# Kernel optimization log

Measured on AMD Instinct MI355X. Metric: run time of the kernel, lower is better.

The kernel has to match this reference:

```python
import jax, jax.numpy as jnp
import numpy as np

N_HEADS = 16


def setup_inputs() -> dict:
    key = jax.random.key(0)
    ks = jax.random.split(key, 5)
    B, T, C = 4, 2048, 1024
    return {
        "x": jax.random.normal(ks[0], (B, T, C), dtype=jnp.float32),
        "W_qkv": jax.random.normal(ks[1], (C, 3 * C), dtype=jnp.float32) * 0.02,
        "b_qkv": jax.random.normal(ks[2], (3 * C,), dtype=jnp.float32) * 0.02,
        "W_proj": jax.random.normal(ks[3], (C, C), dtype=jnp.float32) * 0.02,
        "b_proj": jax.random.normal(ks[4], (C,), dtype=jnp.float32) * 0.02,
    }


def reference(x, W_qkv, b_qkv, W_proj, b_proj):
    B, T, C = x.shape
    H = N_HEADS
    hs = C // H
    # QKV projection. NOTE: original reshapes (B,T,3C) -> (B,T,H,3*hs) then
    # chunks last dim, so q/k/v are interleaved per-head slices of the output.
    qkv = x @ W_qkv + b_qkv                       # [B, T, 3C]
    qkv = qkv.reshape(B, T, H, 3 * hs).transpose(0, 2, 1, 3)  # [B, H, T, 3*hs]
    q, k, v = jnp.split(qkv, 3, axis=-1)          # each [B, H, T, hs]
    scale = 1.0 / (hs ** 0.5)
    scores = jnp.einsum("bhqd,bhkd->bhqk", q, k) * scale  # [B, H, T, T]
    causal = jnp.tril(jnp.ones((T, T), dtype=bool))
    scores = jnp.where(causal, scores, jnp.float32(-1e9))
    attn = jax.nn.softmax(scores, axis=-1)
    out = jnp.einsum("bhqk,bhkd->bhqd", attn, v)  # [B, H, T, hs]
    out = out.transpose(0, 2, 1, 3).reshape(B, T, C)
    return out @ W_proj + b_proj
```

## Files before the change

kernel.cpp:

```cpp
#include <hip/hip_runtime.h>

typedef unsigned short u16;
typedef unsigned int u32;
typedef __attribute__((ext_vector_type(8))) short short8;
typedef __attribute__((ext_vector_type(8))) unsigned short u16x8;
typedef __attribute__((ext_vector_type(4))) unsigned short u16x4;
typedef __attribute__((ext_vector_type(2))) unsigned int u32x2;
typedef __attribute__((ext_vector_type(4))) float f32x4;

__device__ __forceinline__ u16 f2bf(float f){
  u32 u = __builtin_bit_cast(u32, f);
  u32 r = u + 0x7FFFu + ((u >> 16) & 1u);
  return (u16)(r >> 16);
}
__device__ __forceinline__ float bf2f(u16 h){
  u32 u = ((u32)h) << 16;
  return __builtin_bit_cast(float, u);
}
__device__ __forceinline__ float f3max(float a, float b, float c){
  return fmaxf(a, fmaxf(b, c));
}
__device__ __forceinline__ u32 cvtpk(float lo, float hi){
  u32 r;
  asm("v_cvt_pk_bf16_f32 %0, %1, %2" : "=v"(r) : "v"(lo), "v"(hi));
  return r;
}

__device__ __forceinline__ void gld_lds16(const u16* g, u16* l){
  __builtin_amdgcn_global_load_lds(
      (const __attribute__((address_space(1))) u32*)g,
      (__attribute__((address_space(3))) u32*)l, 16, 0, 0);
}

#define MFMA(a,b,c) __builtin_amdgcn_mfma_f32_16x16x32_bf16((a),(b),(c),0,0,0)

__global__ void k_cast_x(const float* __restrict__ in, u16* __restrict__ out, int n8){
  int i = blockIdx.x*256 + threadIdx.x;
  if (i >= n8) return;
  const float4 a = ((const float4*)in)[2*i];
  const float4 b = ((const float4*)in)[2*i+1];
  u16x8 o;
  o[0]=f2bf(a.x); o[1]=f2bf(a.y); o[2]=f2bf(a.z); o[3]=f2bf(a.w);
  o[4]=f2bf(b.x); o[5]=f2bf(b.y); o[6]=f2bf(b.z); o[7]=f2bf(b.w);
  ((u16x8*)out)[i] = o;
}

__global__ void k_transpose_cast(const float* __restrict__ in, u16* __restrict__ out,
                                 int R, int C){
  __shared__ float tile[32][33];
  int c0 = blockIdx.x*32, r0 = blockIdx.y*32;
  int tx = threadIdx.x, ty = threadIdx.y;
  #pragma unroll
  for (int i=0;i<4;i++) tile[ty+8*i][tx] = in[(size_t)(r0+ty+8*i)*C + c0+tx];
  __syncthreads();
  #pragma unroll
  for (int i=0;i<4;i++) out[(size_t)(c0+ty+8*i)*R + r0+tx] = f2bf(tile[tx][ty+8*i]);
}

#define GS_A(T_, BUF) do{                                                      \
  size_t k0_ = (size_t)(T_)*64;                                                \
  _Pragma("unroll")                                                            \
  for (int l=0;l<2;l++){                                                       \
    int r_ = l*64 + (tid>>3);                                                  \
    gld_lds16(Ag + (size_t)(brow + r_)*1024 + k0_ + (((tid&7)^(r_&7))*8),      \
              &Alds[(BUF)*8192 + l*4096 + tid*8]);                             \
  }                                                                            \
}while(0)

#define GS_B(T_, BUF, H_) do{                                                  \
  size_t k0_ = (size_t)(T_)*64;                                                \
  _Pragma("unroll")                                                            \
  for (int l=0;l<2;l++){                                                       \
    int r_ = (H_)*128 + l*64 + (tid>>3);                                       \
    gld_lds16(Bg + (size_t)(bcol + r_)*1024 + k0_ + (((tid&7)^(r_&7))*8),      \
              &Blds[(BUF)*16384 + (H_)*8192 + l*4096 + tid*8]);                \
  }                                                                            \
}while(0)

#define RD_A(MQ, CUR) do{                                                      \
  _Pragma("unroll")                                                            \
  for (int m=0;m<2;m++)                                                        \
    _Pragma("unroll")                                                          \
    for (int k=0;k<2;k++){                                                     \
      int hr = wr*64 + (MQ)*32 + m*16 + lr16;                                  \
      af[(MQ)*2+m][k] = *(const short8*)&Alds[(CUR)*8192 + hr*64 + (((k*4+lg)^(hr&7))*8)]; \
    }                                                                          \
}while(0)

#define RD_B(NQ, CUR) do{                                                      \
  _Pragma("unroll")                                                            \
  for (int n=0;n<2;n++)                                                        \
    _Pragma("unroll")                                                          \
    for (int k=0;k<2;k++){                                                     \
      int hr = wc*64 + (NQ)*32 + n*16 + lr16;                                  \
      bfv[(NQ)*2+n][k] = *(const short8*)&Blds[(CUR)*16384 + hr*64 + (((k*4+lg)^(hr&7))*8)]; \
    }                                                                          \
}while(0)

#define MF8(MQ, NQ)                                                            \
  _Pragma("unroll")                                                            \
  for (int k=0;k<2;k++)                                                        \
    _Pragma("unroll")                                                          \
    for (int m=0;m<2;m++)                                                      \
      _Pragma("unroll")                                                        \
      for (int n=0;n<2;n++)                                                    \
        acc[(MQ)*2+m][(NQ)*2+n] = MFMA(af[(MQ)*2+m][k], bfv[(NQ)*2+n][k], acc[(MQ)*2+m][(NQ)*2+n]);

#define G_TILE(T_, CUR, PF) do{                                                \
  RD_A(0, CUR); RD_B(0, CUR);                                                  \
  if (PF) GS_A((T_)+1, (CUR)^1);                                               \
  __builtin_amdgcn_s_barrier();                                                \
  __builtin_amdgcn_s_setprio(1); MF8(0,0); __builtin_amdgcn_s_setprio(0);      \
  __builtin_amdgcn_s_barrier();                                                \
  RD_B(1, CUR);                                                                \
  if (PF) GS_B((T_)+1, (CUR)^1, 0);                                            \
  __builtin_amdgcn_s_barrier();                                                \
  __builtin_amdgcn_s_setprio(1); MF8(0,1); __builtin_amdgcn_s_setprio(0);      \
  __builtin_amdgcn_s_barrier();                                                \
  RD_A(1, CUR);                                                                \
  if (PF) GS_B((T_)+1, (CUR)^1, 1);                                            \
  __builtin_amdgcn_s_barrier();                                                \
  __builtin_amdgcn_s_setprio(1); MF8(1,1); __builtin_amdgcn_s_setprio(0);      \
  __builtin_amdgcn_s_barrier();                                                \
  __builtin_amdgcn_s_setprio(1); MF8(1,0); __builtin_amdgcn_s_setprio(0);      \
  asm volatile("s_waitcnt vmcnt(0)" ::: "memory");                             \
  __builtin_amdgcn_sched_barrier(0);                                           \
  __builtin_amdgcn_s_barrier();                                                \
}while(0)

template<int OUT_BF16>
__global__ __launch_bounds__(512, 2) void gemm_ph(const u16* __restrict__ Ag,
                                                  const u16* __restrict__ Bg,
                                                  const float* __restrict__ bias,
                                                  void* __restrict__ Cp, int N){
  extern __shared__ u16 lds[];
  u16* Alds = lds;
  u16* Blds = lds + 16384;
  int tid = threadIdx.x, lane = tid&63, wid = tid>>6;
  int wr = wid>>2, wc = wid&3;
  int lr16 = lane&15, lg = lane>>4;
  int nbx = gridDim.x;
  int nwg = nbx*gridDim.y;
  int lin = blockIdx.y*nbx + blockIdx.x;
  int cpx = nwg>>3;
  int swz = (lin&7)*cpx + (lin>>3);
  int bx = swz % nbx, by = swz / nbx;
  size_t brow = (size_t)by*128, bcol = (size_t)bx*256;
  f32x4 acc[4][4] = {};
  short8 af[4][2], bfv[4][2];

  GS_A(0, 0);
  GS_B(0, 0, 0);
  GS_B(0, 0, 1);
  __syncthreads();

  #pragma unroll 1
  for (int kt=0; kt<16; kt+=2){
    G_TILE(kt,   0, true);
    G_TILE(kt+1, 1, (kt+2<16));
  }

  #pragma unroll
  for (int ni=0;ni<4;ni++){
    size_t col = bcol + wc*64 + ni*16 + lr16;
    float bs = bias[col];
    #pragma unroll
    for (int mi=0;mi<4;mi++)
      #pragma unroll
      for (int j=0;j<4;j++){
        size_t row = brow + wr*64 + mi*16 + lg*4 + j;
        float v = acc[mi][ni][j] + bs;
        if (OUT_BF16) ((u16*)Cp)[row*(size_t)N + col] = f2bf(v);
        else          ((float*)Cp)[row*(size_t)N + col] = v;
      }
  }
}

#define ATTN_ITER(KB, CUR, PF) do{                                             \
  int kv0 = (KB)*64;                                                           \
  if (PF){                                                                     \
    int kv1 = kv0 + 64;                                                        \
    va[0] = *(const u16x4*)(qkv + (bt0 + kv1 + vr0    )*3072 + hq + 128 + vd0);\
    va[1] = *(const u16x4*)(qkv + (bt0 + kv1 + vr0 + 1)*3072 + hq + 128 + vd0);\
    gld_lds16(qkv + (bt0+kv1+kr)*3072 + hq + 64 + kcs, &Ks[(CUR)^1][tid*8]);   \
  }                                                                            \
  f32x4 st[4];                                                                 \
  __builtin_amdgcn_s_setprio(1);                                               \
  _Pragma("unroll")                                                            \
  for (int s=0;s<4;s++){                                                       \
    short8 kf0 = *(const short8*)&Ks[CUR][(s*16+lr16)*64 + ((lg  )^rx)*8];     \
    short8 kf1 = *(const short8*)&Ks[CUR][(s*16+lr16)*64 + ((4+lg)^rx)*8];     \
    f32x4 z = {0,0,0,0};                                                       \
    z = MFMA(kf0, qf[0], z);                                                   \
    z = MFMA(kf1, qf[1], z);                                                   \
    st[s] = z;                                                                 \
  }                                                                            \
  __builtin_amdgcn_s_setprio(0);                                               \
  if (kv0 >= qbase){                                                           \
    _Pragma("unroll")                                                          \
    for (int s=0;s<4;s++)                                                      \
      _Pragma("unroll")                                                        \
      for (int j=0;j<4;j++){                                                   \
        int kvg = kv0 + s*16 + lg*4 + j;                                       \
        if (kvg > qglob) st[s][j] = -1e30f;                                    \
      }                                                                        \
  }                                                                            \
  {                                                                            \
    float mx = f3max(st[0][0], st[0][1], st[0][2]);                            \
    mx = f3max(mx, st[0][3], st[1][0]);                                        \
    mx = f3max(mx, st[1][1], st[1][2]);                                        \
    mx = f3max(mx, st[1][3], st[2][0]);                                        \
    mx = f3max(mx, st[2][1], st[2][2]);                                        \
    mx = f3max(mx, st[2][3], st[3][0]);                                        \
    mx = f3max(mx, st[3][1], st[3][2]);                                        \
    mx = fmaxf(mx, st[3][3]);                                                  \
    mx = fmaxf(mx, __shfl_xor(mx, 16));                                        \
    mx = fmaxf(mx, __shfl_xor(mx, 32));                                        \
    if (__any(mx > m_run + 8.f)){                                              \
      float m_new = fmaxf(m_run, mx);                                          \
      float al = exp2f(m_run - m_new);                                         \
      m_run = m_new;                                                           \
      float arow[4];                                                           \
      _Pragma("unroll")                                                        \
      for (int j=0;j<4;j++) arow[j] = __shfl(al, lg*4 + j);                    \
      _Pragma("unroll")                                                        \
      for (int db=0;db<4;db++)                                                 \
        _Pragma("unroll")                                                      \
        for (int j=0;j<4;j++) O[db][j] *= arow[j];                             \
      _Pragma("unroll")                                                        \
      for (int j=0;j<4;j++) acc_l[j] *= arow[j];                               \
    }                                                                          \
    float mr = m_run;                                                          \
    u32 pw[8];                                                                 \
    _Pragma("unroll")                                                          \
    for (int s=0;s<4;s++){                                                     \
      float p0 = exp2f(st[s][0]-mr), p1 = exp2f(st[s][1]-mr);                  \
      float p2 = exp2f(st[s][2]-mr), p3 = exp2f(st[s][3]-mr);                  \
      pw[s*2+0] = cvtpk(p0,p1);                                                \
      pw[s*2+1] = cvtpk(p2,p3);                                                \
    }                                                                          \
    _Pragma("unroll")                                                          \
    for (int s=0;s<4;s++){                                                     \
      int cp = (s*2 + (lg>>1)) ^ rx;                                           \
      u32x2 w2; w2[0] = pw[s*2]; w2[1] = pw[s*2+1];                            \
      *(u32x2*)&Pl[wv][lr16*64 + cp*8 + (lg&1)*4] = w2;                        \
    }                                                                          \
  }                                                                            \
  if (PF){                                                                     \
    _Pragma("unroll")                                                          \
    for (int k=0;k<4;k++){                                                     \
      int d = vd0+k;                                                           \
      int c = (vr0>>3) ^ (d&7) ^ ((d>>3)&7);                                   \
      u32 w = (u32)va[0][k] | ((u32)va[1][k]<<16);                             \
      *(u32*)&Vt[(CUR)^1][d*64 + c*8 + (vr0&7)] = w;                           \
    }                                                                          \
  }                                                                            \
  __builtin_amdgcn_s_setprio(1);                                               \
  _Pragma("unroll")                                                            \
  for (int B=0;B<2;B++){                                                       \
    short8 pa = *(const short8*)&Pl[wv][lr16*64 + (((B<<2)+lg)^rx)*8];         \
    acc_l = MFMA(pa, onesf, acc_l);                                            \
    _Pragma("unroll")                                                          \
    for (int db=0;db<4;db++){                                                  \
      int d = db*16 + lr16;                                                    \
      short8 vf = *(const short8*)&Vt[CUR][d*64 + ((((B<<2)+lg)^(d&7))^((d>>3)&7))*8]; \
      O[db] = MFMA(pa, vf, O[db]);                                             \
    }                                                                          \
  }                                                                            \
  __builtin_amdgcn_s_setprio(0);                                               \
  __syncthreads();                                                             \
}while(0)

__global__ __launch_bounds__(512, 4) void k_attn(const u16* __restrict__ qkv,
                                                 u16* __restrict__ o, int T){
  __shared__ __align__(16) u16 Ks[2][64*64];
  __shared__ __align__(16) u16 Vt[2][64*64];
  __shared__ __align__(16) u16 Pl[8][16*64];
  int tid = threadIdx.x, lane = tid&63, wv = tid>>6;
  int bh = blockIdx.x;
  int b = bh>>4, h = bh&15;
  int hq = h*192;
  size_t bt0 = (size_t)b*T;
  int lr16 = lane&15, lg = lane>>4;
  int rx = lr16&7;
  int vr0 = (tid>>4)*2, vd0 = (tid&15)*4;
  int kr  = tid>>3;
  int kcs = ((tid&7) ^ (kr&7))*8;
  u16x4 va[2];
  const float QS = 0.18033688f;
  u16x8 ov;
  #pragma unroll
  for (int j=0;j<8;j++) ov[j] = 0x3F80;
  const short8 onesf = __builtin_bit_cast(short8, ov);

  #pragma unroll 1
  for (int half=0; half<2; ++half){
    int qt = half ? (int)blockIdx.y : 15 - (int)blockIdx.y;
    int qbase = qt*128;
    short8 qf[2];
    {
      const u16* qp = qkv + (bt0 + qbase + wv*16 + lr16)*3072 + hq + lg*8;
      #pragma unroll
      for (int t=0;t<2;t++){
        u16x8 v = *(const u16x8*)(qp + t*32);
        #pragma unroll
        for (int j=0;j<8;j++) v[j] = f2bf(bf2f(v[j])*QS);
        qf[t] = __builtin_bit_cast(short8, v);
      }
    }
    f32x4 O[4] = {};
    f32x4 acc_l = {0,0,0,0};
    float m_run = -1e30f;
    int qglob = qbase + wv*16 + lr16;

    {
      va[0] = *(const u16x4*)(qkv + (bt0 + vr0    )*3072 + hq + 128 + vd0);
      va[1] = *(const u16x4*)(qkv + (bt0 + vr0 + 1)*3072 + hq + 128 + vd0);
      gld_lds16(qkv + (bt0+kr)*3072 + hq + 64 + kcs, &Ks[0][tid*8]);
      #pragma unroll
      for (int k=0;k<4;k++){
        int d = vd0+k;
        int c = (vr0>>3) ^ (d&7) ^ ((d>>3)&7);
        u32 w = (u32)va[0][k] | ((u32)va[1][k]<<16);
        *(u32*)&Vt[0][d*64 + c*8 + (vr0&7)] = w;
      }
    }
    __syncthreads();

    int nkv = 2*qt + 2;
    #pragma unroll 1
    for (int kb=0; kb<nkv; kb+=2){
      ATTN_ITER(kb,   0, true);
      ATTN_ITER(kb+1, 1, (kb+2<nkv));
    }
    {
      float lrow[4];
      #pragma unroll
      for (int j=0;j<4;j++) lrow[j] = __builtin_amdgcn_rcpf(acc_l[j]);
      #pragma unroll
      for (int db=0;db<4;db++)
        #pragma unroll
        for (int j=0;j<4;j++){
          size_t row = bt0 + qbase + wv*16 + lg*4 + j;
          o[row*1024 + h*64 + db*16 + lr16] = f2bf(O[db][j] * lrow[j]);
        }
    }
  }
}

extern "C" void kernel_launch(void* const* d_in, const int* in_sizes, int n_in,
                              void* d_out, int out_size, void* d_ws, size_t ws_size,
                              hipStream_t stream){
  (void)in_sizes; (void)n_in; (void)out_size; (void)ws_size;
  const float* x     = (const float*)d_in[0];
  const float* Wqkv  = (const float*)d_in[1];
  const float* bqkv  = (const float*)d_in[2];
  const float* Wproj = (const float*)d_in[3];
  const float* bproj = (const float*)d_in[4];
  float* out = (float*)d_out;
  const int B=4, T=2048, C=1024;
  const int M = B*T;
  char* ws = (char*)d_ws;
  u16* qkvb   = (u16*)(ws);
  u16* attnb  = (u16*)(ws + 50331648);
  u16* xb     = (u16*)(ws + 67108864);
  u16* wqkvT  = (u16*)(ws + 83886080);
  u16* wprojT = (u16*)(ws + 90177536);

  k_cast_x<<<4096, 256, 0, stream>>>(x, xb, M*C/8);
  dim3 tb(32,8);
  k_transpose_cast<<<dim3(96,32), tb, 0, stream>>>(Wqkv, wqkvT, C, 3*C);
  k_transpose_cast<<<dim3(32,32), tb, 0, stream>>>(Wproj, wprojT, C, C);
  gemm_ph<1><<<dim3(12,64), 512, 98304, stream>>>(xb, wqkvT, bqkv, qkvb, 3*C);
  k_attn<<<dim3(64,8), 512, 0, stream>>>(qkvb, attnb, T);
  gemm_ph<0><<<dim3(4,64), 512, 98304, stream>>>(attnb, wprojT, bproj, out, C);
}
```

Before: 183.1 us.

## Fuse x fp32-to-bf16 cast into QKV GEMM and widen attention KV tiles

```diff
diff --git a/kernel.cpp b/kernel.cpp
--- a/kernel.cpp
+++ b/kernel.cpp
@@ -6,6 +6,7 @@
 typedef __attribute__((ext_vector_type(8))) unsigned short u16x8;
 typedef __attribute__((ext_vector_type(4))) unsigned short u16x4;
 typedef __attribute__((ext_vector_type(2))) unsigned int u32x2;
+typedef __attribute__((ext_vector_type(4))) unsigned int u32x4;
 typedef __attribute__((ext_vector_type(4))) float f32x4;
 
 __device__ __forceinline__ u16 f2bf(float f){
@@ -33,17 +34,6 @@
 }
 
 #define MFMA(a,b,c) __builtin_amdgcn_mfma_f32_16x16x32_bf16((a),(b),(c),0,0,0)
-
-__global__ void k_cast_x(const float* __restrict__ in, u16* __restrict__ out, int n8){
-  int i = blockIdx.x*256 + threadIdx.x;
-  if (i >= n8) return;
-  const float4 a = ((const float4*)in)[2*i];
-  const float4 b = ((const float4*)in)[2*i+1];
-  u16x8 o;
-  o[0]=f2bf(a.x); o[1]=f2bf(a.y); o[2]=f2bf(a.z); o[3]=f2bf(a.w);
-  o[4]=f2bf(b.x); o[5]=f2bf(b.y); o[6]=f2bf(b.z); o[7]=f2bf(b.w);
-  ((u16x8*)out)[i] = o;
-}
 
 __global__ void k_transpose_cast(const float* __restrict__ in, u16* __restrict__ out,
                                  int R, int C){
@@ -62,8 +52,28 @@
   _Pragma("unroll")                                                            \
   for (int l=0;l<2;l++){                                                       \
     int r_ = l*64 + (tid>>3);                                                  \
-    gld_lds16(Ag + (size_t)(brow + r_)*1024 + k0_ + (((tid&7)^(r_&7))*8),      \
-              &Alds[(BUF)*8192 + l*4096 + tid*8]);                             \
+    size_t off_ = (size_t)(brow + r_)*1024 + k0_ + (((tid&7)^(r_&7))*8);       \
+    if (A_F32){                                                                \
+      fva[l*2]   = *(const float4*)(Agf + off_);                               \
+      fva[l*2+1] = *(const float4*)(Agf + off_ + 4);                           \
+    } else {                                                                   \
+      gld_lds16(Agu + off_, &Alds[(BUF)*8192 + l*4096 + tid*8]);               \
+    }                                                                          \
+  }                                                                            \
+}while(0)
+
+#define GS_A_COMMIT(BUF) do{                                                   \
+  if (A_F32){                                                                  \
+    _Pragma("unroll")                                                          \
+    for (int l=0;l<2;l++){                                                     \
+      u32x4 wv4;                                                               \
+      wv4[0]=cvtpk(fva[l*2].x,  fva[l*2].y);                                   \
+      wv4[1]=cvtpk(fva[l*2].z,  fva[l*2].w);                                   \
+      wv4[2]=cvtpk(fva[l*2+1].x,fva[l*2+1].y);                                 \
+      wv4[3]=cvtpk(fva[l*2+1].z,fva[l*2+1].w);                                 \
+      *(u32x4*)&Alds[(BUF)*8192 + l*4096 + tid*8] = wv4;                       \
+    }                                                                          \
+    asm volatile("s_waitcnt lgkmcnt(0)" ::: "memory");                         \
   }                                                                            \
 }while(0)
 
@@ -124,18 +134,22 @@
   __builtin_amdgcn_s_barrier();                                                \
   __builtin_amdgcn_s_setprio(1); MF8(1,0); __builtin_amdgcn_s_setprio(0);      \
   asm volatile("s_waitcnt vmcnt(0)" ::: "memory");                             \
+  if (PF) GS_A_COMMIT((CUR)^1);                                                \
   __builtin_amdgcn_sched_barrier(0);                                           \
   __builtin_amdgcn_s_barrier();                                                \
 }while(0)
 
-template<int OUT_BF16>
-__global__ __launch_bounds__(512, 2) void gemm_ph(const u16* __restrict__ Ag,
+template<int OUT_BF16, int A_F32>
+__global__ __launch_bounds__(512, 2) void gemm_ph(const void* __restrict__ Ag,
                                                   const u16* __restrict__ Bg,
                                                   const float* __restrict__ bias,
                                                   void* __restrict__ Cp, int N){
   extern __shared__ u16 lds[];
   u16* Alds = lds;
   u16* Blds = lds + 16384;
+  const u16* Agu = (const u16*)Ag;
+  const float* Agf = (const float*)Ag;
+  float4 fva[4];
   int tid = threadIdx.x, lane = tid&63, wid = tid>>6;
   int wr = wid>>2, wc = wid&3;
   int lr16 = lane&15, lg = lane>>4;
@@ -152,6 +166,7 @@
   GS_A(0, 0);
   GS_B(0, 0, 0);
   GS_B(0, 0, 1);
+  GS_A_COMMIT(0);
   __syncthreads();
 
   #pragma unroll 1
@@ -176,33 +191,28 @@
   }
 }
 
-#define ATTN_ITER(KB, CUR, PF) do{                                             \
-  int kv0 = (KB)*64;                                                           \
-  if (PF){                                                                     \
-    int kv1 = kv0 + 64;                                                        \
-    va[0] = *(const u16x4*)(qkv + (bt0 + kv1 + vr0    )*3072 + hq + 128 + vd0);\
-    va[1] = *(const u16x4*)(qkv + (bt0 + kv1 + vr0 + 1)*3072 + hq + 128 + vd0);\
-    gld_lds16(qkv + (bt0+kv1+kr)*3072 + hq + 64 + kcs, &Ks[(CUR)^1][tid*8]);   \
-  }                                                                            \
+#define ATTN_SUB(S, CUR) do{                                                   \
   f32x4 st[4];                                                                 \
   __builtin_amdgcn_s_setprio(1);                                               \
   _Pragma("unroll")                                                            \
-  for (int s=0;s<4;s++){                                                       \
-    short8 kf0 = *(const short8*)&Ks[CUR][(s*16+lr16)*64 + ((lg  )^rx)*8];     \
-    short8 kf1 = *(const short8*)&Ks[CUR][(s*16+lr16)*64 + ((4+lg)^rx)*8];     \
+  for (int sb=0;sb<4;sb++){                                                    \
+    int row = (S)*64 + sb*16 + lr16;                                           \
+    short8 kf0 = *(const short8*)&Ks[CUR][row*64 + ((lg  )^rx)*8];             \
+    short8 kf1 = *(const short8*)&Ks[CUR][row*64 + ((4+lg)^rx)*8];             \
     f32x4 z = {0,0,0,0};                                                       \
     z = MFMA(kf0, qf[0], z);                                                   \
     z = MFMA(kf1, qf[1], z);                                                   \
-    st[s] = z;                                                                 \
+    st[sb] = z;                                                                \
   }                                                                            \
   __builtin_amdgcn_s_setprio(0);                                               \
+  int kv0 = kvt + (S)*64;                                                      \
   if (kv0 >= qbase){                                                           \
     _Pragma("unroll")                                                          \
-    for (int s=0;s<4;s++)                                                      \
+    for (int sb=0;sb<4;sb++)                                                   \
       _Pragma("unroll")                                                        \
       for (int j=0;j<4;j++){                                                   \
-        int kvg = kv0 + s*16 + lg*4 + j;                                       \
-        if (kvg > qglob) st[s][j] = -1e30f;                                    \
+        int kvg = kv0 + sb*16 + lg*4 + j;                                      \
+        if (kvg > qglob) st[sb][j] = -1e30f;                                   \
       }                                                                        \
   }                                                                            \
   {                                                                            \
@@ -233,48 +243,65 @@
     float mr = m_run;                                                          \
     u32 pw[8];                                                                 \
     _Pragma("unroll")                                                          \
-    for (int s=0;s<4;s++){                                                     \
-      float p0 = exp2f(st[s][0]-mr), p1 = exp2f(st[s][1]-mr);                  \
-      float p2 = exp2f(st[s][2]-mr), p3 = exp2f(st[s][3]-mr);                  \
-      pw[s*2+0] = cvtpk(p0,p1);                                                \
-      pw[s*2+1] = cvtpk(p2,p3);                                                \
-    }                                                                          \
-    _Pragma("unroll")                                                          \
-    for (int s=0;s<4;s++){                                                     \
-      int cp = (s*2 + (lg>>1)) ^ rx;                                           \
-      u32x2 w2; w2[0] = pw[s*2]; w2[1] = pw[s*2+1];                            \
+    for (int sb=0;sb<4;sb++){                                                  \
+      float p0 = exp2f(st[sb][0]-mr), p1 = exp2f(st[sb][1]-mr);                \
+      float p2 = exp2f(st[sb][2]-mr), p3 = exp2f(st[sb][3]-mr);                \
+      pw[sb*2+0] = cvtpk(p0,p1);                                               \
+      pw[sb*2+1] = cvtpk(p2,p3);                                               \
+    }                                                                          \
+    _Pragma("unroll")                                                          \
+    for (int sb=0;sb<4;sb++){                                                  \
+      int cp = (sb*2 + (lg>>1)) ^ rx;                                          \
+      u32x2 w2; w2[0] = pw[sb*2]; w2[1] = pw[sb*2+1];                          \
       *(u32x2*)&Pl[wv][lr16*64 + cp*8 + (lg&1)*4] = w2;                        \
     }                                                                          \
   }                                                                            \
+  __builtin_amdgcn_s_setprio(1);                                               \
+  _Pragma("unroll")                                                            \
+  for (int B=0;B<2;B++){                                                       \
+    short8 pa = *(const short8*)&Pl[wv][lr16*64 + (((B<<2)+lg)^rx)*8];         \
+    acc_l = MFMA(pa, onesf, acc_l);                                            \
+    _Pragma("unroll")                                                          \
+    for (int db=0;db<4;db++){                                                  \
+      int d = db*16 + lr16;                                                    \
+      short8 vf = *(const short8*)&Vt[d*128 + ((S)*8 + (((B<<2)+lg)^((d&7)^((d>>3)&7))))*8]; \
+      O[db] = MFMA(pa, vf, O[db]);                                             \
+    }                                                                          \
+  }                                                                            \
+  __builtin_amdgcn_s_setprio(0);                                               \
+}while(0)
+
+#define ATTN_TILE(T_, CUR, PF) do{                                             \
+  int kvt = (T_)*128;                                                          \
+  if (PF){                                                                     \
+    int kv1 = kvt + 128;                                                       \
+    _Pragma("unroll")                                                          \
+    for (int i=0;i<4;i++)                                                      \
+      va[i] = *(const u16x4*)(qkv + (bt0 + kv1 + vr0 + i)*3072 + hq + 128 + vd0); \
+    gld_lds16(qkv + (bt0+kv1+kr)*3072 + hq + 64 + kcs, &Ks[(CUR)^1][tid*8]);   \
+    gld_lds16(qkv + (bt0+kv1+64+kr)*3072 + hq + 64 + kcs, &Ks[(CUR)^1][4096 + tid*8]); \
+  }                                                                            \
+  ATTN_SUB(0, CUR);                                                            \
+  ATTN_SUB(1, CUR);                                                            \
+  __builtin_amdgcn_s_barrier();                                                \
   if (PF){                                                                     \
     _Pragma("unroll")                                                          \
     for (int k=0;k<4;k++){                                                     \
       int d = vd0+k;                                                           \
       int c = (vr0>>3) ^ (d&7) ^ ((d>>3)&7);                                   \
-      u32 w = (u32)va[0][k] | ((u32)va[1][k]<<16);                             \
-      *(u32*)&Vt[(CUR)^1][d*64 + c*8 + (vr0&7)] = w;                           \
-    }                                                                          \
-  }                                                                            \
-  __builtin_amdgcn_s_setprio(1);                                               \
-  _Pragma("unroll")                                                            \
-  for (int B=0;B<2;B++){                                                       \
-    short8 pa = *(const short8*)&Pl[wv][lr16*64 + (((B<<2)+lg)^rx)*8];         \
-    acc_l = MFMA(pa, onesf, acc_l);                                            \
-    _Pragma("unroll")                                                          \
-    for (int db=0;db<4;db++){                                                  \
-      int d = db*16 + lr16;                                                    \
-      short8 vf = *(const short8*)&Vt[CUR][d*64 + ((((B<<2)+lg)^(d&7))^((d>>3)&7))*8]; \
-      O[db] = MFMA(pa, vf, O[db]);                                             \
-    }                                                                          \
-  }                                                                            \
-  __builtin_amdgcn_s_setprio(0);                                               \
+      u32x2 w;                                                                 \
+      w[0] = (u32)va[0][k] | ((u32)va[1][k]<<16);                              \
+      w[1] = (u32)va[2][k] | ((u32)va[3][k]<<16);                              \
+      *(u32x2*)&Vt[d*128 + c*8 + (vr0&7)] = w;                                 \
+    }                                                                          \
+  }                                                                            \
   __syncthreads();                                                             \
 }while(0)
 
 __global__ __launch_bounds__(512, 4) void k_attn(const u16* __restrict__ qkv,
                                                  u16* __restrict__ o, int T){
-  __shared__ __align__(16) u16 Ks[2][64*64];
-  __shared__ __align__(16) u16 Vt[2][64*64];
+  __shared__ __align__(16) u16 Ks[2][128*64];
+  __shared__ __align__(16) u16 Vt[64*128];
   __shared__ __align__(16) u16 Pl[8][16*64];
   int tid = threadIdx.x, lane = tid&63, wv = tid>>6;
   int bh = blockIdx.x;
@@ -283,10 +310,10 @@
   size_t bt0 = (size_t)b*T;
   int lr16 = lane&15, lg = lane>>4;
   int rx = lr16&7;
-  int vr0 = (tid>>4)*2, vd0 = (tid&15)*4;
+  int vr0 = (tid>>4)*4, vd0 = (tid&15)*4;
   int kr  = tid>>3;
   int kcs = ((tid&7) ^ (kr&7))*8;
-  u16x4 va[2];
+  u16x4 va[4];
   const float QS = 0.18033688f;
   u16x8 ov;
   #pragma unroll
@@ -314,25 +341,32 @@
     int qglob = qbase + wv*16 + lr16;
 
     {
-      va[0] = *(const u16x4*)(qkv + (bt0 + vr0    )*3072 + hq + 128 + vd0);
-      va[1] = *(const u16x4*)(qkv + (bt0 + vr0 + 1)*3072 + hq + 128 + vd0);
+      #pragma unroll
+      for (int i=0;i<4;i++)
+        va[i] = *(const u16x4*)(qkv + (bt0 + vr0 + i)*3072 + hq + 128 + vd0);
       gld_lds16(qkv + (bt0+kr)*3072 + hq + 64 + kcs, &Ks[0][tid*8]);
+      gld_lds16(qkv + (bt0+64+kr)*3072 + hq + 64 + kcs, &Ks[0][4096 + tid*8]);
       #pragma unroll
       for (int k=0;k<4;k++){
         int d = vd0+k;
         int c = (vr0>>3) ^ (d&7) ^ ((d>>3)&7);
-        u32 w = (u32)va[0][k] | ((u32)va[1][k]<<16);
-        *(u32*)&Vt[0][d*64 + c*8 + (vr0&7)] = w;
+        u32x2 w;
+        w[0] = (u32)va[0][k] | ((u32)va[1][k]<<16);
+        w[1] = (u32)va[2][k] | ((u32)va[3][k]<<16);
+        *(u32x2*)&Vt[d*128 + c*8 + (vr0&7)] = w;
       }
     }
     __syncthreads();
 
-    int nkv = 2*qt + 2;
+    int nt = qt + 1;
+    int t = 0;
     #pragma unroll 1
-    for (int kb=0; kb<nkv; kb+=2){
-      ATTN_ITER(kb,   0, true);
-      ATTN_ITER(kb+1, 1, (kb+2<nkv));
+    for (; t+1 < nt; t += 2){
+      ATTN_TILE(t,   0, true);
+      ATTN_TILE(t+1, 1, (t+2<nt));
     }
+    if (t < nt) ATTN_TILE(t, 0, false);
+
     {
       float lrow[4];
       #pragma unroll
@@ -359,19 +393,17 @@
   const float* bproj = (const float*)d_in[4];
   float* out = (float*)d_out;
   const int B=4, T=2048, C=1024;
-  const int M = B*T;
+  (void)B;
   char* ws = (char*)d_ws;
   u16* qkvb   = (u16*)(ws);
   u16* attnb  = (u16*)(ws + 50331648);
-  u16* xb     = (u16*)(ws + 67108864);
   u16* wqkvT  = (u16*)(ws + 83886080);
   u16* wprojT = (u16*)(ws + 90177536);
 
-  k_cast_x<<<4096, 256, 0, stream>>>(x, xb, M*C/8);
   dim3 tb(32,8);
   k_transpose_cast<<<dim3(96,32), tb, 0, stream>>>(Wqkv, wqkvT, C, 3*C);
   k_transpose_cast<<<dim3(32,32), tb, 0, stream>>>(Wproj, wprojT, C, C);
-  gemm_ph<1><<<dim3(12,64), 512, 98304, stream>>>(xb, wqkvT, bqkv, qkvb, 3*C);
+  gemm_ph<1,1><<<dim3(12,64), 512, 98304, stream>>>((const void*)x, wqkvT, bqkv, qkvb, 3*C);
   k_attn<<<dim3(64,8), 512, 0, stream>>>(qkvb, attnb, T);
-  gemm_ph<0><<<dim3(4,64), 512, 98304, stream>>>(attnb, wprojT, bproj, out, C);
-}
+  gemm_ph<0,0><<<dim3(4,64), 512, 98304, stream>>>((const void*)attnb, wprojT, bproj, out, C);
+}
```

Measured after the change: 209.8 us. +14.6%, slower.

## Fuse fp32-to-bf16 cast of x into QKV GEMM A-tile loads

Applied to the files above, without the earlier changes.

```diff
diff --git a/kernel.cpp b/kernel.cpp
--- a/kernel.cpp
+++ b/kernel.cpp
@@ -6,6 +6,7 @@
 typedef __attribute__((ext_vector_type(8))) unsigned short u16x8;
 typedef __attribute__((ext_vector_type(4))) unsigned short u16x4;
 typedef __attribute__((ext_vector_type(2))) unsigned int u32x2;
+typedef __attribute__((ext_vector_type(4))) unsigned int u32x4;
 typedef __attribute__((ext_vector_type(4))) float f32x4;
 
 __device__ __forceinline__ u16 f2bf(float f){
@@ -33,17 +34,6 @@
 }
 
 #define MFMA(a,b,c) __builtin_amdgcn_mfma_f32_16x16x32_bf16((a),(b),(c),0,0,0)
-
-__global__ void k_cast_x(const float* __restrict__ in, u16* __restrict__ out, int n8){
-  int i = blockIdx.x*256 + threadIdx.x;
-  if (i >= n8) return;
-  const float4 a = ((const float4*)in)[2*i];
-  const float4 b = ((const float4*)in)[2*i+1];
-  u16x8 o;
-  o[0]=f2bf(a.x); o[1]=f2bf(a.y); o[2]=f2bf(a.z); o[3]=f2bf(a.w);
-  o[4]=f2bf(b.x); o[5]=f2bf(b.y); o[6]=f2bf(b.z); o[7]=f2bf(b.w);
-  ((u16x8*)out)[i] = o;
-}
 
 __global__ void k_transpose_cast(const float* __restrict__ in, u16* __restrict__ out,
                                  int R, int C){
@@ -62,8 +52,28 @@
   _Pragma("unroll")                                                            \
   for (int l=0;l<2;l++){                                                       \
     int r_ = l*64 + (tid>>3);                                                  \
-    gld_lds16(Ag + (size_t)(brow + r_)*1024 + k0_ + (((tid&7)^(r_&7))*8),      \
-              &Alds[(BUF)*8192 + l*4096 + tid*8]);                             \
+    size_t off_ = (size_t)(brow + r_)*1024 + k0_ + (((tid&7)^(r_&7))*8);       \
+    if (A_F32){                                                                \
+      fva[l*2]   = *(const float4*)(Agf + off_);                               \
+      fva[l*2+1] = *(const float4*)(Agf + off_ + 4);                           \
+    } else {                                                                   \
+      gld_lds16(Agu + off_, &Alds[(BUF)*8192 + l*4096 + tid*8]);               \
+    }                                                                          \
+  }                                                                            \
+}while(0)
+
+#define GS_A_COMMIT(BUF) do{                                                   \
+  if (A_F32){                                                                  \
+    _Pragma("unroll")                                                          \
+    for (int l=0;l<2;l++){                                                     \
+      u32x4 wv4;                                                               \
+      wv4[0]=cvtpk(fva[l*2].x,  fva[l*2].y);                                   \
+      wv4[1]=cvtpk(fva[l*2].z,  fva[l*2].w);                                   \
+      wv4[2]=cvtpk(fva[l*2+1].x,fva[l*2+1].y);                                 \
+      wv4[3]=cvtpk(fva[l*2+1].z,fva[l*2+1].w);                                 \
+      *(u32x4*)&Alds[(BUF)*8192 + l*4096 + tid*8] = wv4;                       \
+    }                                                                          \
+    asm volatile("s_waitcnt lgkmcnt(0)" ::: "memory");                         \
   }                                                                            \
 }while(0)
 
@@ -124,18 +134,22 @@
   __builtin_amdgcn_s_barrier();                                                \
   __builtin_amdgcn_s_setprio(1); MF8(1,0); __builtin_amdgcn_s_setprio(0);      \
   asm volatile("s_waitcnt vmcnt(0)" ::: "memory");                             \
+  if (PF) GS_A_COMMIT((CUR)^1);                                                \
   __builtin_amdgcn_sched_barrier(0);                                           \
   __builtin_amdgcn_s_barrier();                                                \
 }while(0)
 
-template<int OUT_BF16>
-__global__ __launch_bounds__(512, 2) void gemm_ph(const u16* __restrict__ Ag,
+template<int OUT_BF16, int A_F32>
+__global__ __launch_bounds__(512, 2) void gemm_ph(const void* __restrict__ Ag,
                                                   const u16* __restrict__ Bg,
                                                   const float* __restrict__ bias,
                                                   void* __restrict__ Cp, int N){
   extern __shared__ u16 lds[];
   u16* Alds = lds;
   u16* Blds = lds + 16384;
+  const u16* Agu = (const u16*)Ag;
+  const float* Agf = (const float*)Ag;
+  float4 fva[4];
   int tid = threadIdx.x, lane = tid&63, wid = tid>>6;
   int wr = wid>>2, wc = wid&3;
   int lr16 = lane&15, lg = lane>>4;
@@ -152,6 +166,7 @@
   GS_A(0, 0);
   GS_B(0, 0, 0);
   GS_B(0, 0, 1);
+  GS_A_COMMIT(0);
   __syncthreads();
 
   #pragma unroll 1
@@ -359,19 +374,17 @@
   const float* bproj = (const float*)d_in[4];
   float* out = (float*)d_out;
   const int B=4, T=2048, C=1024;
-  const int M = B*T;
+  (void)B;
   char* ws = (char*)d_ws;
   u16* qkvb   = (u16*)(ws);
   u16* attnb  = (u16*)(ws + 50331648);
-  u16* xb     = (u16*)(ws + 67108864);
   u16* wqkvT  = (u16*)(ws + 83886080);
   u16* wprojT = (u16*)(ws + 90177536);
 
-  k_cast_x<<<4096, 256, 0, stream>>>(x, xb, M*C/8);
   dim3 tb(32,8);
   k_transpose_cast<<<dim3(96,32), tb, 0, stream>>>(Wqkv, wqkvT, C, 3*C);
   k_transpose_cast<<<dim3(32,32), tb, 0, stream>>>(Wproj, wprojT, C, C);
-  gemm_ph<1><<<dim3(12,64), 512, 98304, stream>>>(xb, wqkvT, bqkv, qkvb, 3*C);
+  gemm_ph<1,1><<<dim3(12,64), 512, 98304, stream>>>((const void*)x, wqkvT, bqkv, qkvb, 3*C);
   k_attn<<<dim3(64,8), 512, 0, stream>>>(qkvb, attnb, T);
-  gemm_ph<0><<<dim3(4,64), 512, 98304, stream>>>(attnb, wprojT, bproj, out, C);
-}
+  gemm_ph<0,0><<<dim3(4,64), 512, 98304, stream>>>((const void*)attnb, wprojT, bproj, out, C);
+}
```

Result: no change. 185.6 us (+1.4%).
